# Kernel tuning notes

Measured on AMD Instinct MI355X. Metric: run time of the kernel, lower is better.

The kernel has to match this reference:

```python
import jax, jax.numpy as jnp
import numpy as np
import math

D = 1024
H = 16
S = 2048

def setup_inputs() -> dict:
    key = jax.random.key(0)
    k1, k2, k3 = jax.random.split(key, 3)
    x = jax.random.normal(k1, (2, S, D), dtype=jnp.float32)
    # nn.Linear(D, 3D): weight [3D, D], bias [3D]
    W = jax.random.normal(k2, (3 * D, D), dtype=jnp.float32) / math.sqrt(D)
    b = jax.random.normal(k3, (3 * D,), dtype=jnp.float32) * 0.01
    return {"x": x, "W": W, "b": b}

def reference(x, W, b):
    N, C, Dm = x.shape
    hd = Dm // H
    z = jnp.einsum('ncd,ed->nce', x, W) + b  # [N, C, 3D]
    k = z[:, :, :Dm].reshape(N, C, H, hd).transpose(0, 2, 1, 3)
    q = z[:, :, Dm:2 * Dm].reshape(N, C, H, hd).transpose(0, 2, 1, 3)
    v = z[:, :, 2 * Dm:].reshape(N, C, H, hd).transpose(0, 2, 1, 3)
    # NOTE: original scales by 1/sqrt(D) (full dim), not 1/sqrt(head_dim)
    scores = jnp.einsum('nhqd,nhkd->nhqk', q, k) / math.sqrt(Dm)
    causal = jnp.tril(jnp.ones((C, C), dtype=bool))
    scores = jnp.where(causal[None, None], scores, -jnp.inf)
    attn = jax.nn.softmax(scores, axis=-1)
    out = jnp.einsum('nhqk,nhkd->nhqd', attn, v)
    return out.transpose(0, 2, 1, 3).reshape(N, C, Dm)
```

## Files before the change

### kernel.cpp

```cpp
#include <hip/hip_runtime.h>
#include <hip/hip_bf16.h>

#define D_MODEL 1024
#define NH 16
#define HD 64
#define S_LEN 2048
#define NB 2
#define M_TOT 4096
#define N3 3072

typedef __attribute__((ext_vector_type(8))) short bf16x8;
typedef __attribute__((ext_vector_type(4))) float f32x4;
typedef __attribute__((ext_vector_type(4))) unsigned short u16x4;

__device__ __forceinline__ unsigned short f2bf(float f) {
    unsigned int u = __float_as_uint(f);
    u += 0x7fffu + ((u >> 16) & 1u);
    return (unsigned short)(u >> 16);
}

#define GLOAD_LDS(gp, lp)                                                      \
    __builtin_amdgcn_global_load_lds(                                          \
        (const __attribute__((address_space(1))) void*)(gp),                   \
        (__attribute__((address_space(3))) void*)(lp), 16, 0, 0)

__global__ __launch_bounds__(256) void cast_f32_bf16(
    const float* __restrict__ in, unsigned short* __restrict__ out, int n4) {
    int i = blockIdx.x * 256 + threadIdx.x;
    if (i < n4) {
        float4 v = reinterpret_cast<const float4*>(in)[i];
        u16x4 o;
        o.x = f2bf(v.x); o.y = f2bf(v.y); o.z = f2bf(v.z); o.w = f2bf(v.w);
        reinterpret_cast<u16x4*>(out)[i] = o;
    }
}

#define BM 128
#define BN 128
#define BK 64

__global__ __launch_bounds__(256) void qkv_gemm(
    const unsigned short* __restrict__ A, const unsigned short* __restrict__ B,
    const float* __restrict__ bias, unsigned short* __restrict__ Z) {
    __shared__ unsigned short As[BM * BK];
    __shared__ unsigned short Bs[BN * BK];

    const int t = threadIdx.x;
    const int lane = t & 63;
    const int wid = t >> 6;
    const int wr = wid >> 1, wc = wid & 1;
    const int bm = blockIdx.y, bn = blockIdx.x;
    const int lr = lane & 15;
    const int lg = lane >> 4;
    const int srow = lane >> 3;
    const int sslot = lane & 7;

    f32x4 acc[4][4] = {};

    for (int k0 = 0; k0 < 1024; k0 += BK) {
        __syncthreads();
#pragma unroll
        for (int p = 0; p < 4; ++p) {
            int rb = wid * 32 + p * 8;
            int row = rb + srow;
            int seg = sslot ^ (row & 7);
            GLOAD_LDS(&A[(size_t)(bm * BM + row) * 1024 + k0 + seg * 8],
                      &As[rb * BK]);
            GLOAD_LDS(&B[(size_t)(bn * BN + row) * 1024 + k0 + seg * 8],
                      &Bs[rb * BK]);
        }
        __syncthreads();
#pragma unroll
        for (int ks = 0; ks < 2; ++ks) {
            bf16x8 af[4], bfr[4];
#pragma unroll
            for (int m = 0; m < 4; ++m) {
                int row = wr * 64 + m * 16 + lr;
                int slot = (ks * 4 + lg) ^ (row & 7);
                af[m] = *reinterpret_cast<const bf16x8*>(&As[row * BK + slot * 8]);
            }
#pragma unroll
            for (int n = 0; n < 4; ++n) {
                int row = wc * 64 + n * 16 + lr;
                int slot = (ks * 4 + lg) ^ (row & 7);
                bfr[n] = *reinterpret_cast<const bf16x8*>(&Bs[row * BK + slot * 8]);
            }
#pragma unroll
            for (int m = 0; m < 4; ++m)
#pragma unroll
                for (int n = 0; n < 4; ++n)
                    acc[m][n] = __builtin_amdgcn_mfma_f32_16x16x32_bf16(
                        af[m], bfr[n], acc[m][n], 0, 0, 0);
        }
    }
#pragma unroll
    for (int m = 0; m < 4; ++m) {
        int row = bm * BM + wr * 64 + m * 16 + lg * 4;
#pragma unroll
        for (int n = 0; n < 4; ++n) {
            int col = bn * BN + wc * 64 + n * 16 + lr;
            float bv = bias[col];
#pragma unroll
            for (int i = 0; i < 4; ++i) {
                Z[(size_t)(row + i) * N3 + col] = f2bf(acc[m][n][i] + bv);
            }
        }
    }
}

__global__ __launch_bounds__(256) void transpose_v(
    const unsigned short* __restrict__ Z, unsigned short* __restrict__ Vt) {
    __shared__ unsigned short tile[64][72];
    int bid = blockIdx.x;
    int nh = bid >> 5;
    int cb = bid & 31;
    int n = nh >> 4, h = nh & 15;
    int t = threadIdx.x;
#pragma unroll
    for (int p = 0; p < 4; ++p) {
        int idx = p * 256 + t;
        int r = idx >> 4;
        int cg = idx & 15;
        u16x4 v = *reinterpret_cast<const u16x4*>(
            &Z[(size_t)(n * S_LEN + cb * 64 + r) * N3 + 2 * D_MODEL + h * HD + cg * 4]);
        *reinterpret_cast<u16x4*>(&tile[r][cg * 4]) = v;
    }
    __syncthreads();
#pragma unroll
    for (int p = 0; p < 4; ++p) {
        int idx = p * 256 + t;
        int d = idx >> 4;
        int cg = idx & 15;
        u16x4 o;
        o.x = tile[cg * 4 + 0][d];
        o.y = tile[cg * 4 + 1][d];
        o.z = tile[cg * 4 + 2][d];
        o.w = tile[cg * 4 + 3][d];
        *reinterpret_cast<u16x4*>(
            &Vt[((size_t)nh * 64 + d) * S_LEN + cb * 64 + cg * 4]) = o;
    }
}

__global__ __launch_bounds__(256) void attn(
    const unsigned short* __restrict__ Z, const unsigned short* __restrict__ Vt,
    float* __restrict__ Out) {
    const int ilin = blockIdx.y * 32 + blockIdx.x;
    const int head32 = (ilin & 7) * 4 + ((ilin >> 3) & 3);
    const int qb = 31 - (ilin >> 5);
    const int n = head32 >> 4, h = head32 & 15;

    __shared__ unsigned short Kt[2][64 * 64];
    __shared__ unsigned short Vs[2][64 * 64];
    __shared__ unsigned short p_lds[4][16][72];

    const int t = threadIdx.x;
    const int lane = t & 63, w = t >> 6;
    const int lr = lane & 15, lg = lane >> 4;
    const int srow = lane >> 3, sslot = lane & 7;

    const size_t zrowQ = (size_t)(n * S_LEN + qb * 64 + w * 16 + lr) * N3 + D_MODEL + h * HD;
    bf16x8 qf[2];
    qf[0] = *reinterpret_cast<const bf16x8*>(&Z[zrowQ + lg * 8]);
    qf[1] = *reinterpret_cast<const bf16x8*>(&Z[zrowQ + 32 + lg * 8]);

    auto STAGE = [&](int buf, int kb) {
#pragma unroll
        for (int p = 0; p < 2; ++p) {
            int rb = w * 16 + p * 8;
            int row = rb + srow;
            int seg = sslot ^ (row & 7);
            GLOAD_LDS(&Z[(size_t)(n * S_LEN + kb * 64 + row) * N3 + h * HD + seg * 8],
                      &Kt[buf][rb * 64]);
            GLOAD_LDS(&Vt[((size_t)head32 * 64 + row) * S_LEN + kb * 64 + seg * 8],
                      &Vs[buf][rb * 64]);
        }
    };

    f32x4 o[4] = {};
    float mrun[4], lrun[4];
#pragma unroll
    for (int i = 0; i < 4; ++i) { mrun[i] = -1e30f; lrun[i] = 0.f; }

    const int qrow_base = qb * 64 + w * 16 + lg * 4;

    STAGE(0, 0);
    int cur = 0;
    for (int kb = 0; kb <= qb; ++kb) {
        __syncthreads();
        if (kb < qb) STAGE(cur ^ 1, kb + 1);
        const unsigned short* Kc = &Kt[cur][0];
        const unsigned short* Vc = &Vs[cur][0];

        f32x4 s[4];
#pragma unroll
        for (int cf = 0; cf < 4; ++cf) {
            int row = cf * 16 + lr;
            bf16x8 kf0 = *reinterpret_cast<const bf16x8*>(
                &Kc[row * 64 + ((lg) ^ (row & 7)) * 8]);
            bf16x8 kf1 = *reinterpret_cast<const bf16x8*>(
                &Kc[row * 64 + ((lg + 4) ^ (row & 7)) * 8]);
            f32x4 a = {};
            a = __builtin_amdgcn_mfma_f32_16x16x32_bf16(qf[0], kf0, a, 0, 0, 0);
            a = __builtin_amdgcn_mfma_f32_16x16x32_bf16(qf[1], kf1, a, 0, 0, 0);
            s[cf] = a;
        }
        const bool diag = (kb == qb);
#pragma unroll
        for (int cf = 0; cf < 4; ++cf) {
            int kcol = kb * 64 + cf * 16 + lr;
#pragma unroll
            for (int i = 0; i < 4; ++i) {
                float v = s[cf][i] * 0.03125f;
                if (diag && kcol > qrow_base + i) v = -1e30f;
                s[cf][i] = v;
            }
        }
#pragma unroll
        for (int i = 0; i < 4; ++i) {
            float v = fmaxf(fmaxf(s[0][i], s[1][i]), fmaxf(s[2][i], s[3][i]));
            v = fmaxf(v, __shfl_xor(v, 1));
            v = fmaxf(v, __shfl_xor(v, 2));
            v = fmaxf(v, __shfl_xor(v, 4));
            v = fmaxf(v, __shfl_xor(v, 8));
            float mn = fmaxf(mrun[i], v);
            float corr = __expf(mrun[i] - mn);
            mrun[i] = mn;
            float sum = 0.f;
#pragma unroll
            for (int cf = 0; cf < 4; ++cf) {
                float p = __expf(s[cf][i] - mn);
                s[cf][i] = p;
                sum += p;
            }
            sum += __shfl_xor(sum, 1);
            sum += __shfl_xor(sum, 2);
            sum += __shfl_xor(sum, 4);
            sum += __shfl_xor(sum, 8);
            lrun[i] = lrun[i] * corr + sum;
#pragma unroll
            for (int cfd = 0; cfd < 4; ++cfd) o[cfd][i] *= corr;
        }
#pragma unroll
        for (int cf = 0; cf < 4; ++cf)
#pragma unroll
            for (int i = 0; i < 4; ++i)
                p_lds[w][lg * 4 + i][cf * 16 + lr] = f2bf(s[cf][i]);
#pragma unroll
        for (int ks = 0; ks < 2; ++ks) {
            bf16x8 pf = *reinterpret_cast<const bf16x8*>(&p_lds[w][lr][ks * 32 + lg * 8]);
#pragma unroll
            for (int cfd = 0; cfd < 4; ++cfd) {
                int vrow = cfd * 16 + lr;
                bf16x8 vf = *reinterpret_cast<const bf16x8*>(
                    &Vc[vrow * 64 + ((ks * 4 + lg) ^ (vrow & 7)) * 8]);
                o[cfd] = __builtin_amdgcn_mfma_f32_16x16x32_bf16(pf, vf, o[cfd], 0, 0, 0);
            }
        }
        cur ^= 1;
    }
#pragma unroll
    for (int cfd = 0; cfd < 4; ++cfd) {
        int d = h * HD + cfd * 16 + lr;
#pragma unroll
        for (int i = 0; i < 4; ++i) {
            int q = qb * 64 + w * 16 + lg * 4 + i;
            Out[(size_t)(n * S_LEN + q) * D_MODEL + d] = o[cfd][i] / lrun[i];
        }
    }
}

extern "C" void kernel_launch(void* const* d_in, const int* in_sizes, int n_in,
                              void* d_out, int out_size, void* d_ws, size_t ws_size,
                              hipStream_t stream) {
    const float* x = (const float*)d_in[0];
    const float* W = (const float*)d_in[1];
    const float* b = (const float*)d_in[2];
    float* out = (float*)d_out;

    char* ws = (char*)d_ws;
    unsigned short* xb = (unsigned short*)ws;
    unsigned short* Wb = (unsigned short*)(ws + (size_t)8 * 1024 * 1024);
    unsigned short* Z  = (unsigned short*)(ws + (size_t)14 * 1024 * 1024);
    unsigned short* Vt = (unsigned short*)(ws + (size_t)38 * 1024 * 1024);

    cast_f32_bf16<<<4096, 256, 0, stream>>>(x, xb, M_TOT * D_MODEL / 4);
    cast_f32_bf16<<<3072, 256, 0, stream>>>(W, Wb, N3 * D_MODEL / 4);
    qkv_gemm<<<dim3(N3 / BN, M_TOT / BM), 256, 0, stream>>>(xb, Wb, b, Z);
    transpose_v<<<1024, 256, 0, stream>>>(Z, Vt);
    attn<<<dim3(S_LEN / 64, NB * NH), 256, 0, stream>>>(Z, Vt, out);
}
```

Baseline: 189.1 us.

## Process two query tiles per attention block and merge the cast kernels

Each attention workgroup now handles 128 query rows as two 64-row groups, so every staged K/V tile serves both groups. This halves K/V global loads per query and halves the number of blocks. The softmax moves to exp2 with the log2e factor folded into the scale, and it skips the rescale of the running max when the new max exceeds it by no more than 8. It also adds s_setprio around the MFMA sections and a launch bound of three waves per block, and merges the two f32-to-bf16 cast launches into one. The costs are more registers per thread, fewer blocks to hide latency, and a lazy rescale that relies on fp32 headroom for accuracy.

Result: slower. 221.7 us (+17.2%).

```diff
diff --git a/kernel.cpp b/kernel.cpp
--- a/kernel.cpp
+++ b/kernel.cpp
@@ -24,15 +24,21 @@
         (const __attribute__((address_space(1))) void*)(gp),                   \
         (__attribute__((address_space(3))) void*)(lp), 16, 0, 0)
 
-__global__ __launch_bounds__(256) void cast_f32_bf16(
-    const float* __restrict__ in, unsigned short* __restrict__ out, int n4) {
+__global__ __launch_bounds__(256) void cast_both(
+    const float* __restrict__ x, const float* __restrict__ W,
+    unsigned short* __restrict__ xb, unsigned short* __restrict__ Wb) {
+    const int nx = M_TOT * D_MODEL / 4;
+    const int nw = N3 * D_MODEL / 4;
     int i = blockIdx.x * 256 + threadIdx.x;
-    if (i < n4) {
-        float4 v = reinterpret_cast<const float4*>(in)[i];
-        u16x4 o;
-        o.x = f2bf(v.x); o.y = f2bf(v.y); o.z = f2bf(v.z); o.w = f2bf(v.w);
-        reinterpret_cast<u16x4*>(out)[i] = o;
-    }
+    const float* src;
+    unsigned short* dst;
+    int j;
+    if (i < nx) { src = x; dst = xb; j = i; }
+    else { j = i - nx; if (j >= nw) return; src = W; dst = Wb; }
+    float4 v = reinterpret_cast<const float4*>(src)[j];
+    u16x4 o;
+    o.x = f2bf(v.x); o.y = f2bf(v.y); o.z = f2bf(v.z); o.w = f2bf(v.w);
+    reinterpret_cast<u16x4*>(dst)[j] = o;
 }
 
 #define BM 128
@@ -141,27 +147,31 @@
     }
 }
 
-__global__ __launch_bounds__(256) void attn(
+__global__ __launch_bounds__(256, 3) void attn(
     const unsigned short* __restrict__ Z, const unsigned short* __restrict__ Vt,
     float* __restrict__ Out) {
-    const int ilin = blockIdx.y * 32 + blockIdx.x;
+    const int ilin = blockIdx.y * 16 + blockIdx.x;
     const int head32 = (ilin & 7) * 4 + ((ilin >> 3) & 3);
-    const int qb = 31 - (ilin >> 5);
+    const int qb = 15 - (ilin >> 5);
     const int n = head32 >> 4, h = head32 & 15;
 
     __shared__ unsigned short Kt[2][64 * 64];
     __shared__ unsigned short Vs[2][64 * 64];
-    __shared__ unsigned short p_lds[4][16][72];
+    __shared__ unsigned short p_lds[4][32][72];
 
     const int t = threadIdx.x;
     const int lane = t & 63, w = t >> 6;
     const int lr = lane & 15, lg = lane >> 4;
     const int srow = lane >> 3, sslot = lane & 7;
 
-    const size_t zrowQ = (size_t)(n * S_LEN + qb * 64 + w * 16 + lr) * N3 + D_MODEL + h * HD;
-    bf16x8 qf[2];
-    qf[0] = *reinterpret_cast<const bf16x8*>(&Z[zrowQ + lg * 8]);
-    qf[1] = *reinterpret_cast<const bf16x8*>(&Z[zrowQ + 32 + lg * 8]);
+    bf16x8 qf[2][2];
+#pragma unroll
+    for (int g = 0; g < 2; ++g) {
+        const size_t zrowQ =
+            (size_t)(n * S_LEN + qb * 128 + g * 64 + w * 16 + lr) * N3 + D_MODEL + h * HD;
+        qf[g][0] = *reinterpret_cast<const bf16x8*>(&Z[zrowQ + lg * 8]);
+        qf[g][1] = *reinterpret_cast<const bf16x8*>(&Z[zrowQ + 32 + lg * 8]);
+    }
 
     auto STAGE = [&](int buf, int kb) {
 #pragma unroll
@@ -176,97 +186,130 @@
         }
     };
 
-    f32x4 o[4] = {};
-    float mrun[4], lrun[4];
-#pragma unroll
-    for (int i = 0; i < 4; ++i) { mrun[i] = -1e30f; lrun[i] = 0.f; }
-
-    const int qrow_base = qb * 64 + w * 16 + lg * 4;
+    f32x4 o[2][4] = {};
+    float mrun[2][4], lrun[2][4];
+#pragma unroll
+    for (int g = 0; g < 2; ++g)
+#pragma unroll
+        for (int i = 0; i < 4; ++i) { mrun[g][i] = -1e30f; lrun[g][i] = 0.f; }
+
+    const float SCL = 0.03125f * 1.44269504f;
+    const int nkb = 2 * qb + 2;
 
     STAGE(0, 0);
     int cur = 0;
-    for (int kb = 0; kb <= qb; ++kb) {
+    for (int kb = 0; kb < nkb; ++kb) {
         __syncthreads();
-        if (kb < qb) STAGE(cur ^ 1, kb + 1);
+        if (kb + 1 < nkb) STAGE(cur ^ 1, kb + 1);
         const unsigned short* Kc = &Kt[cur][0];
         const unsigned short* Vc = &Vs[cur][0];
 
-        f32x4 s[4];
+        bf16x8 kf0[4], kf1[4];
 #pragma unroll
         for (int cf = 0; cf < 4; ++cf) {
             int row = cf * 16 + lr;
-            bf16x8 kf0 = *reinterpret_cast<const bf16x8*>(
+            kf0[cf] = *reinterpret_cast<const bf16x8*>(
                 &Kc[row * 64 + ((lg) ^ (row & 7)) * 8]);
-            bf16x8 kf1 = *reinterpret_cast<const bf16x8*>(
+            kf1[cf] = *reinterpret_cast<const bf16x8*>(
                 &Kc[row * 64 + ((lg + 4) ^ (row & 7)) * 8]);
-            f32x4 a = {};
-            a = __builtin_amdgcn_mfma_f32_16x16x32_bf16(qf[0], kf0, a, 0, 0, 0);
-            a = __builtin_amdgcn_mfma_f32_16x16x32_bf16(qf[1], kf1, a, 0, 0, 0);
-            s[cf] = a;
-        }
-        const bool diag = (kb == qb);
-#pragma unroll
-        for (int cf = 0; cf < 4; ++cf) {
-            int kcol = kb * 64 + cf * 16 + lr;
+        }
+
+#pragma unroll
+        for (int g = 0; g < 2; ++g) {
+            if (kb > 2 * qb + g) continue;
+            f32x4 s[4];
+            __builtin_amdgcn_s_setprio(1);
+#pragma unroll
+            for (int cf = 0; cf < 4; ++cf) {
+                f32x4 a = {};
+                a = __builtin_amdgcn_mfma_f32_16x16x32_bf16(qf[g][0], kf0[cf], a, 0, 0, 0);
+                a = __builtin_amdgcn_mfma_f32_16x16x32_bf16(qf[g][1], kf1[cf], a, 0, 0, 0);
+                s[cf] = a;
+            }
+            __builtin_amdgcn_s_setprio(0);
+            const bool diag = (kb == 2 * qb + g);
+#pragma unroll
+            for (int cf = 0; cf < 4; ++cf) {
+                int krel = cf * 16 + lr;
+#pragma unroll
+                for (int i = 0; i < 4; ++i) {
+                    float v = s[cf][i] * SCL;
+                    if (diag && krel > w * 16 + lg * 4 + i) v = -1e30f;
+                    s[cf][i] = v;
+                }
+            }
+            float pm[4];
 #pragma unroll
             for (int i = 0; i < 4; ++i) {
-                float v = s[cf][i] * 0.03125f;
-                if (diag && kcol > qrow_base + i) v = -1e30f;
-                s[cf][i] = v;
-            }
-        }
-#pragma unroll
-        for (int i = 0; i < 4; ++i) {
-            float v = fmaxf(fmaxf(s[0][i], s[1][i]), fmaxf(s[2][i], s[3][i]));
-            v = fmaxf(v, __shfl_xor(v, 1));
-            v = fmaxf(v, __shfl_xor(v, 2));
-            v = fmaxf(v, __shfl_xor(v, 4));
-            v = fmaxf(v, __shfl_xor(v, 8));
-            float mn = fmaxf(mrun[i], v);
-            float corr = __expf(mrun[i] - mn);
-            mrun[i] = mn;
-            float sum = 0.f;
-#pragma unroll
-            for (int cf = 0; cf < 4; ++cf) {
-                float p = __expf(s[cf][i] - mn);
-                s[cf][i] = p;
-                sum += p;
-            }
-            sum += __shfl_xor(sum, 1);
-            sum += __shfl_xor(sum, 2);
-            sum += __shfl_xor(sum, 4);
-            sum += __shfl_xor(sum, 8);
-            lrun[i] = lrun[i] * corr + sum;
-#pragma unroll
-            for (int cfd = 0; cfd < 4; ++cfd) o[cfd][i] *= corr;
-        }
-#pragma unroll
-        for (int cf = 0; cf < 4; ++cf)
-#pragma unroll
-            for (int i = 0; i < 4; ++i)
-                p_lds[w][lg * 4 + i][cf * 16 + lr] = f2bf(s[cf][i]);
-#pragma unroll
-        for (int ks = 0; ks < 2; ++ks) {
-            bf16x8 pf = *reinterpret_cast<const bf16x8*>(&p_lds[w][lr][ks * 32 + lg * 8]);
-#pragma unroll
-            for (int cfd = 0; cfd < 4; ++cfd) {
-                int vrow = cfd * 16 + lr;
-                bf16x8 vf = *reinterpret_cast<const bf16x8*>(
-                    &Vc[vrow * 64 + ((ks * 4 + lg) ^ (vrow & 7)) * 8]);
-                o[cfd] = __builtin_amdgcn_mfma_f32_16x16x32_bf16(pf, vf, o[cfd], 0, 0, 0);
-            }
+                float v = fmaxf(fmaxf(s[0][i], s[1][i]), fmaxf(s[2][i], s[3][i]));
+                v = fmaxf(v, __shfl_xor(v, 1));
+                v = fmaxf(v, __shfl_xor(v, 2));
+                v = fmaxf(v, __shfl_xor(v, 4));
+                v = fmaxf(v, __shfl_xor(v, 8));
+                pm[i] = v;
+            }
+            float worst = fmaxf(fmaxf(pm[0] - mrun[g][0], pm[1] - mrun[g][1]),
+                                fmaxf(pm[2] - mrun[g][2], pm[3] - mrun[g][3]));
+            if (!__all(worst <= 8.0f)) {
+#pragma unroll
+                for (int i = 0; i < 4; ++i) {
+                    float mn = fmaxf(mrun[g][i], pm[i]);
+                    float corr = exp2f(mrun[g][i] - mn);
+                    mrun[g][i] = mn;
+                    lrun[g][i] *= corr;
+#pragma unroll
+                    for (int cfd = 0; cfd < 4; ++cfd) o[g][cfd][i] *= corr;
+                }
+            }
+#pragma unroll
+            for (int i = 0; i < 4; ++i) {
+                float sum = 0.f;
+#pragma unroll
+                for (int cf = 0; cf < 4; ++cf) {
+                    float p = exp2f(s[cf][i] - mrun[g][i]);
+                    s[cf][i] = p;
+                    sum += p;
+                }
+                sum += __shfl_xor(sum, 1);
+                sum += __shfl_xor(sum, 2);
+                sum += __shfl_xor(sum, 4);
+                sum += __shfl_xor(sum, 8);
+                lrun[g][i] += sum;
+            }
+#pragma unroll
+            for (int cf = 0; cf < 4; ++cf)
+#pragma unroll
+                for (int i = 0; i < 4; ++i)
+                    p_lds[w][g * 16 + lg * 4 + i][cf * 16 + lr] = f2bf(s[cf][i]);
+            __builtin_amdgcn_s_setprio(1);
+#pragma unroll
+            for (int ks = 0; ks < 2; ++ks) {
+                bf16x8 pf = *reinterpret_cast<const bf16x8*>(
+                    &p_lds[w][g * 16 + lr][ks * 32 + lg * 8]);
+#pragma unroll
+                for (int cfd = 0; cfd < 4; ++cfd) {
+                    int vrow = cfd * 16 + lr;
+                    bf16x8 vf = *reinterpret_cast<const bf16x8*>(
+                        &Vc[vrow * 64 + ((ks * 4 + lg) ^ (vrow & 7)) * 8]);
+                    o[g][cfd] = __builtin_amdgcn_mfma_f32_16x16x32_bf16(
+                        pf, vf, o[g][cfd], 0, 0, 0);
+                }
+            }
+            __builtin_amdgcn_s_setprio(0);
         }
         cur ^= 1;
     }
 #pragma unroll
-    for (int cfd = 0; cfd < 4; ++cfd) {
-        int d = h * HD + cfd * 16 + lr;
-#pragma unroll
-        for (int i = 0; i < 4; ++i) {
-            int q = qb * 64 + w * 16 + lg * 4 + i;
-            Out[(size_t)(n * S_LEN + q) * D_MODEL + d] = o[cfd][i] / lrun[i];
-        }
-    }
+    for (int g = 0; g < 2; ++g)
+#pragma unroll
+        for (int cfd = 0; cfd < 4; ++cfd) {
+            int d = h * HD + cfd * 16 + lr;
+#pragma unroll
+            for (int i = 0; i < 4; ++i) {
+                int q = qb * 128 + g * 64 + w * 16 + lg * 4 + i;
+                Out[(size_t)(n * S_LEN + q) * D_MODEL + d] = o[g][cfd][i] / lrun[g][i];
+            }
+        }
 }
 
 extern "C" void kernel_launch(void* const* d_in, const int* in_sizes, int n_in,
@@ -283,9 +326,8 @@
     unsigned short* Z  = (unsigned short*)(ws + (size_t)14 * 1024 * 1024);
     unsigned short* Vt = (unsigned short*)(ws + (size_t)38 * 1024 * 1024);
 
-    cast_f32_bf16<<<4096, 256, 0, stream>>>(x, xb, M_TOT * D_MODEL / 4);
-    cast_f32_bf16<<<3072, 256, 0, stream>>>(W, Wb, N3 * D_MODEL / 4);
+    cast_both<<<7168, 256, 0, stream>>>(x, W, xb, Wb);
     qkv_gemm<<<dim3(N3 / BN, M_TOT / BM), 256, 0, stream>>>(xb, Wb, b, Z);
     transpose_v<<<1024, 256, 0, stream>>>(Z, Vt);
-    attn<<<dim3(S_LEN / 64, NB * NH), 256, 0, stream>>>(Z, Vt, out);
-}
+    attn<<<dim3(16, 32), 256, 0, stream>>>(Z, Vt, out);
+}
```
